# Kernel tuning notes

Hardware: AMD Instinct MI355X
Metric: run time of the kernel (lower is better)

The kernel has to match this reference:

```python
import jax, jax.numpy as jnp
import numpy as np

KRYLOV_DIM = 8
T_END = 1.0
EPS = 1e-12


def setup_inputs() -> dict:
    key = jax.random.key(0)
    k1, k2, k3 = jax.random.split(key, 3)
    B, C, H, Wd = 8, 256, 64, 64
    s0 = jax.random.uniform(k1, (B, C, H, Wd), dtype=jnp.float32)
    v = jax.random.normal(k2, (B, C, H, Wd), dtype=jnp.float32)
    W = jax.random.normal(k3, (C, C), dtype=jnp.float32) / np.float32(np.sqrt(C))
    return {"s0": s0, "v": v, "W": W}


def reference(s0, v, W):
    # fitness: learned channel-mixing linear operator (1x1-conv style)
    def fitness(x):
        return jnp.einsum('oc,bchw->bohw', W, x)

    # replicator vector field R_{s}[x] = s*x - s * sum_c(s*x)
    def replicator(s, x):
        sx = s * x
        return sx - s * jnp.sum(sx, axis=1, keepdims=True)

    A = lambda x: fitness(replicator(s0, x))
    dot = lambda a, b: jnp.sum(a * b, axis=(1, 2, 3))  # batched inner product

    m = KRYLOV_DIM
    B = v.shape[0]

    # ---- Arnoldi iteration (batched, modified Gram-Schmidt) ----
    vnorm = jnp.sqrt(dot(v, v))  # [B]
    Q = [v / vnorm[:, None, None, None]]
    Hcols = []
    for k in range(m):
        w = A(Q[k])
        col = []
        for j in range(k + 1):
            h = dot(Q[j], w)               # [B]
            col.append(h)
            w = w - h[:, None, None, None] * Q[j]
        hnext = jnp.sqrt(dot(w, w))        # subdiagonal entry
        Q.append(w / (hnext + EPS)[:, None, None, None])
        col.append(hnext)
        col += [jnp.zeros_like(hnext)] * (m - k - 1)  # pad column to m+1 rows
        Hcols.append(jnp.stack(col, axis=-1))          # [B, m+1]
    Hmat = jnp.stack(Hcols, axis=-1)  # [B, m+1, m]
    T = Hmat[:, :m, :]                # square upper-Hessenberg [B, m, m]

    # ---- extended matrix + batched small matrix exponential ----
    ext = jnp.zeros((B, m + 1, m + 1), dtype=T.dtype)
    ext = ext.at[:, :m, :m].set(T_END * T)
    ext = ext.at[:, 0, m].set(T_END)
    expm_ext = jax.scipy.linalg.expm(ext)   # batched over leading dim
    coords = expm_ext[:, :m, -1]            # [B, m] Krylov coordinates

    # ---- fused weighted sum of Krylov vectors ----
    Qstack = jnp.stack(Q[:m], axis=0)       # [m, B, C, H, W]
    v_end = jnp.einsum('bj,jbchw->bchw', coords, Qstack)
    return v_end * vnorm[:, None, None, None]
```

## Files before the change

kernel.cpp:

```cpp
#include <hip/hip_runtime.h>
#include <math.h>

#define Bn   8
#define Cn   256
#define HWn  4096
#define FB   (Cn * HWn)
#define NTOT (Bn * FB)
#define TEND 1.0
#define EPSK 1e-12f
#define NT   64
#define RS   56
#define WTS  68

typedef float f32x4 __attribute__((ext_vector_type(4)));
typedef short bf16x8 __attribute__((ext_vector_type(8)));

__device__ inline float b2f(unsigned int u) {
    return __uint_as_float(u << 16);
}
__device__ inline unsigned short f2b(float f) {
    unsigned u = __float_as_uint(f);
    unsigned r = u + 0x7FFFu + ((u >> 16) & 1u);
    return (unsigned short)(r >> 16);
}


__global__ void init_kernel(float* __restrict__ p) {
    for (int i = threadIdx.x; i < 1024; i += 256) p[i] = 0.0f;
}

__global__ void wsplit_kernel(const float* __restrict__ W,
                              unsigned short* __restrict__ Whs,
                              unsigned short* __restrict__ Wls) {
    int kc = blockIdx.x, mt = blockIdx.y, l = threadIdx.x;
    int m = mt * 16 + (l & 15);
    int k0 = kc * 32 + (l >> 4) * 8;
#pragma unroll
    for (int j = 0; j < 8; ++j) {
        float wv = W[m * 256 + k0 + j];
        unsigned short h = f2b(wv);
        unsigned short lo = f2b(wv - b2f(h));
        int idx = ((kc * 16 + mt) * 64 + l) * 8 + j;
        Whs[idx] = h; Wls[idx] = lo;
    }
}

template <int K>
__global__ __launch_bounds__(256, 3) void step_kernel(
        const float* __restrict__ v, const float* __restrict__ s0,
        const unsigned short* __restrict__ Whs, const unsigned short* __restrict__ Wls,
        unsigned short* __restrict__ Qb, float* __restrict__ acc,
        float* __restrict__ w) {
    __shared__ __align__(16) char smem_u[34816];
    short* Ph   = (short*)smem_u;
    short* Pl   = (short*)(smem_u + 7168);
    float* tred = (float*)(smem_u + 14336);
    float* wt   = (float*)smem_u;
    __shared__ float ts[NT];
    __shared__ float nred[4];
    __shared__ float dred[4][8];
    const int tid = threadIdx.x;
    const int b = blockIdx.y;
    const int sbase = blockIdx.x * NT;
    const size_t boff = (size_t)b * FB;
    const int lane = tid & 63, wvi = tid >> 6;
    const int mbase = wvi * 64;
    const int cg = tid >> 4;
    const int pos = (tid & 15) * 4;

    float cj[K > 0 ? K : 1];
    if (K > 0) {
        float mm[K > 0 ? K : 1];
        mm[0] = sqrtf(acc[512 + b]);
#pragma unroll
        for (int j = 1; j < K; ++j) mm[j] = sqrtf(acc[512 + j * 8 + b]) + EPSK * mm[j - 1];
#pragma unroll
        for (int j = 0; j < K; ++j)
            cj[j] = acc[((K - 1) * 8 + j) * 8 + b] / (mm[j] * mm[j]);
    }
    unsigned short* QK = Qb + (size_t)(K > 0 ? K - 1 : 0) * NTOT;

    float tp[4] = {0.f, 0.f, 0.f, 0.f};
    float np = 0.f;
#pragma unroll 4
    for (int cc = 0; cc < 16; ++cc) {
        int c = cc * 16 + cg;
        size_t off = boff + (size_t)c * HWn + sbase + pos;
        float4 sv = *(const float4*)(s0 + off);
        float se[4] = {sv.x, sv.y, sv.z, sv.w};
        if (K == 0) {
            float4 xv = *(const float4*)(v + off);
            float xe[4] = {xv.x, xv.y, xv.z, xv.w};
#pragma unroll
            for (int i = 0; i < 4; ++i) {
                np = fmaf(xe[i], xe[i], np);
                tp[i] = fmaf(xe[i], se[i], tp[i]);
            }
        } else {
            float4 wv4 = *(const float4*)(w + off);
            float4 vv4 = *(const float4*)(v + off);
            float xe[4];
            xe[0] = fmaf(-cj[0], vv4.x, wv4.x);
            xe[1] = fmaf(-cj[0], vv4.y, wv4.y);
            xe[2] = fmaf(-cj[0], vv4.z, wv4.z);
            xe[3] = fmaf(-cj[0], vv4.w, wv4.w);
#pragma unroll
            for (int j = 1; j < K; ++j) {
                ushort4 u = *(const ushort4*)(Qb + (size_t)(j - 1) * NTOT + off);
                xe[0] = fmaf(-cj[j], b2f(u.x), xe[0]);
                xe[1] = fmaf(-cj[j], b2f(u.y), xe[1]);
                xe[2] = fmaf(-cj[j], b2f(u.z), xe[2]);
                xe[3] = fmaf(-cj[j], b2f(u.w), xe[3]);
            }
            unsigned int h0 = f2b(xe[0]), h1 = f2b(xe[1]);
            unsigned int h2 = f2b(xe[2]), h3 = f2b(xe[3]);
            ushort4 o;
            o.x = (unsigned short)h0; o.y = (unsigned short)h1;
            o.z = (unsigned short)h2; o.w = (unsigned short)h3;
            *(ushort4*)(QK + off) = o;
            float xr[4] = {b2f(h0), b2f(h1), b2f(h2), b2f(h3)};
#pragma unroll
            for (int i = 0; i < 4; ++i) {
                np = fmaf(xr[i], xr[i], np);
                tp[i] = fmaf(xr[i], se[i], tp[i]);
            }
        }
    }
    for (int off2 = 32; off2 > 0; off2 >>= 1) np += __shfl_down(np, off2);
    if (lane == 0) nred[wvi] = np;
    *(float4*)(tred + cg * WTS + pos) = *(float4*)tp;
    __syncthreads();
    if (tid < 64) {
        float s = 0.f;
#pragma unroll
        for (int g = 0; g < 16; ++g) s += tred[g * WTS + tid];
        ts[tid] = s;
    }
    if (tid == 0)
        atomicAdd(&acc[512 + K * 8 + b], nred[0] + nred[1] + nred[2] + nred[3]);
    __syncthreads();

    f32x4 ac[4][4];
#pragma unroll
    for (int i = 0; i < 4; ++i)
#pragma unroll
        for (int j = 0; j < 4; ++j) ac[i][j] = (f32x4){0.f, 0.f, 0.f, 0.f};

    for (int kc = 0; kc < 8; ++kc) {
        __syncthreads();
#pragma unroll
        for (int ci = 0; ci < 2; ++ci) {
            int cl = ci * 16 + cg;
            int c = kc * 32 + cl;
            size_t off = boff + (size_t)c * HWn + sbase + pos;
            float4 sv = *(const float4*)(s0 + off);
            float se[4] = {sv.x, sv.y, sv.z, sv.w};
            float xr[4];
            if (K == 0) {
                float4 xv = *(const float4*)(v + off);
                xr[0] = xv.x; xr[1] = xv.y; xr[2] = xv.z; xr[3] = xv.w;
            } else {
                ushort4 u = *(const ushort4*)(QK + off);
                xr[0] = b2f(u.x); xr[1] = b2f(u.y); xr[2] = b2f(u.z); xr[3] = b2f(u.w);
            }
#pragma unroll
            for (int i = 0; i < 4; ++i) {
                float p = se[i] * (xr[i] - ts[pos + i]);
                unsigned short h = f2b(p);
                unsigned short l = f2b(p - b2f(h));
                Ph[(pos + i) * RS + cl] = (short)h;
                Pl[(pos + i) * RS + cl] = (short)l;
            }
        }
        __syncthreads();
        bf16x8 ah[4], al[4], bh[4], bl[4];
#pragma unroll
        for (int rt = 0; rt < 4; ++rt) {
            int mt = (mbase >> 4) + rt;
            ah[rt] = *(const bf16x8*)(Whs + (size_t)kc * 8192 + (mt * 64 + lane) * 8);
            al[rt] = *(const bf16x8*)(Wls + (size_t)kc * 8192 + (mt * 64 + lane) * 8);
        }
#pragma unroll
        for (int ct = 0; ct < 4; ++ct) {
            int n = ct * 16 + (lane & 15);
            int k8 = (lane >> 4) * 8;
            bh[ct] = *(bf16x8*)(Ph + n * RS + k8);
            bl[ct] = *(bf16x8*)(Pl + n * RS + k8);
        }
#pragma unroll
        for (int rt = 0; rt < 4; ++rt)
#pragma unroll
            for (int ct = 0; ct < 4; ++ct) {
                ac[rt][ct] = __builtin_amdgcn_mfma_f32_16x16x32_bf16(ah[rt], bh[ct], ac[rt][ct], 0, 0, 0);
                ac[rt][ct] = __builtin_amdgcn_mfma_f32_16x16x32_bf16(ah[rt], bl[ct], ac[rt][ct], 0, 0, 0);
                ac[rt][ct] = __builtin_amdgcn_mfma_f32_16x16x32_bf16(al[rt], bh[ct], ac[rt][ct], 0, 0, 0);
            }
    }

    float dp[K + 1];
#pragma unroll
    for (int j = 0; j <= K; ++j) dp[j] = 0.f;
#pragma unroll
    for (int g = 0; g < 2; ++g) {
        __syncthreads();
        if ((wvi >> 1) == g) {
            int rl = (wvi & 1) * 64;
#pragma unroll
            for (int rt = 0; rt < 4; ++rt)
#pragma unroll
                for (int ct = 0; ct < 4; ++ct) {
                    int r0 = rl + rt * 16 + (lane >> 4) * 4;
                    int ccol = ct * 16 + (lane & 15);
#pragma unroll
                    for (int reg = 0; reg < 4; ++reg)
                        wt[(r0 + reg) * WTS + ccol] = ac[rt][ct][reg];
                }
        }
        __syncthreads();
#pragma unroll
        for (int rr = 0; rr < 8; ++rr) {
            int rlocal = rr * 16 + (tid >> 4);
            int rabs = g * 128 + rlocal;
            int col = (tid & 15) * 4;
            const float* src = wt + rlocal * WTS + col;
            float4 wv4 = {src[0], src[1], src[2], src[3]};
            size_t idx = boff + (size_t)rabs * HWn + sbase + col;
            *(float4*)(w + idx) = wv4;
            float4 vv4 = *(const float4*)(v + idx);
            dp[0] = fmaf(wv4.x, vv4.x, dp[0]);
            dp[0] = fmaf(wv4.y, vv4.y, dp[0]);
            dp[0] = fmaf(wv4.z, vv4.z, dp[0]);
            dp[0] = fmaf(wv4.w, vv4.w, dp[0]);
#pragma unroll
            for (int j = 1; j <= K; ++j) {
                ushort4 u = *(const ushort4*)(Qb + (size_t)(j - 1) * NTOT + idx);
                dp[j] = fmaf(wv4.x, b2f(u.x), dp[j]);
                dp[j] = fmaf(wv4.y, b2f(u.y), dp[j]);
                dp[j] = fmaf(wv4.z, b2f(u.z), dp[j]);
                dp[j] = fmaf(wv4.w, b2f(u.w), dp[j]);
            }
        }
    }
#pragma unroll
    for (int j = 0; j <= K; ++j) {
        float q = dp[j];
        for (int off2 = 32; off2 > 0; off2 >>= 1) q += __shfl_down(q, off2);
        if (lane == 0) dred[wvi][j] = q;
    }
    __syncthreads();
    if (tid <= K)
        atomicAdd(&acc[(K * 8 + tid) * 8 + b],
                  dred[0][tid] + dred[1][tid] + dred[2][tid] + dred[3][tid]);
}

__global__ __launch_bounds__(128) void expm_kernel(const float* __restrict__ acc,
                                                   float* __restrict__ coordsOut) {
    __shared__ double Am[81], Pm[81], Tm[81];
    __shared__ double ssc;
    __shared__ int sn;
    const int b = blockIdx.x;
    const int t = threadIdx.x;
    const int r = t / 9, c = t % 9;
    double m[8];
    m[0] = sqrt((double)acc[512 + b]);
    for (int j = 1; j < 8; ++j) m[j] = sqrt((double)acc[512 + j * 8 + b]) + 1e-12 * m[j - 1];
    if (t < 81) {
        double val = 0.0;
        if (r < 8 && c < 8) {
            if (r <= c) val = TEND * (double)acc[(c * 8 + r) * 8 + b] / (m[r] * m[c]);
            else if (r == c + 1) val = TEND * sqrt((double)acc[512 + r * 8 + b]) / m[c];
        }
        if (r == 0 && c == 8) val = TEND;
        Am[t] = val;
    }
    __syncthreads();
    if (t == 0) {
        double mx = 0.0;
        for (int rr = 0; rr < 9; ++rr) {
            double s = 0.0;
            for (int cc = 0; cc < 9; ++cc) s += fabs(Am[rr * 9 + cc]);
            if (s > mx) mx = s;
        }
        int n = 0;
        while (mx > 0.25 && n < 48) { mx *= 0.5; ++n; }
        double sc = 1.0;
        for (int ii = 0; ii < n; ++ii) sc *= 0.5;
        sn = n; ssc = sc;
    }
    __syncthreads();
    if (t < 81) Am[t] *= ssc;
    __syncthreads();
    if (t < 81) Pm[t] = (r == c) ? 1.0 : 0.0;
    __syncthreads();
    for (int i = 20; i >= 1; --i) {
        if (t < 81) {
            double s = 0.0;
            for (int k = 0; k < 9; ++k) s += Am[r * 9 + k] * Pm[k * 9 + c];
            Tm[t] = ((r == c) ? 1.0 : 0.0) + s / (double)i;
        }
        __syncthreads();
        if (t < 81) Pm[t] = Tm[t];
        __syncthreads();
    }
    int n = sn;
    for (int q = 0; q < n; ++q) {
        if (t < 81) {
            double s = 0.0;
            for (int k = 0; k < 9; ++k) s += Pm[r * 9 + k] * Pm[k * 9 + c];
            Tm[t] = s;
        }
        __syncthreads();
        if (t < 81) Pm[t] = Tm[t];
        __syncthreads();
    }
    if (t < 8) coordsOut[b * 8 + t] = (float)(Pm[t * 9 + 8] * m[0] / m[t]);
}

__device__ inline void unp8(uint4 u, float* f) {
    f[0] = b2f(u.x & 0xFFFFu); f[1] = b2f(u.x >> 16);
    f[2] = b2f(u.y & 0xFFFFu); f[3] = b2f(u.y >> 16);
    f[4] = b2f(u.z & 0xFFFFu); f[5] = b2f(u.z >> 16);
    f[6] = b2f(u.w & 0xFFFFu); f[7] = b2f(u.w >> 16);
}

__global__ __launch_bounds__(256) void combine_kernel(const unsigned short* __restrict__ Qb,
                                                      const float* __restrict__ v,
                                                      const float* __restrict__ coords,
                                                      float* __restrict__ out) {
    int b = blockIdx.y;
    const size_t boff = (size_t)b * FB;
    float cf[8];
#pragma unroll
    for (int j = 0; j < 8; ++j) cf[j] = coords[b * 8 + j];
    const float4* vv = (const float4*)(v + boff);
    const uint4* uv[8];
#pragma unroll
    for (int j = 1; j < 8; ++j)
        uv[j] = (const uint4*)(Qb + (size_t)(j - 1) * NTOT + boff);
    int i = blockIdx.x * 256 + threadIdx.x;
    float4* ov = (float4*)(out + boff);
#pragma unroll
    for (int r = 0; r < 2; ++r) {
        int idx = i + r * 65536;
        float4 v0 = vv[2 * idx], v1 = vv[2 * idx + 1];
        float a[8] = {cf[0] * v0.x, cf[0] * v0.y, cf[0] * v0.z, cf[0] * v0.w,
                      cf[0] * v1.x, cf[0] * v1.y, cf[0] * v1.z, cf[0] * v1.w};
#pragma unroll
        for (int j = 1; j < 8; ++j) {
            uint4 u = uv[j][idx];
            float ue[8]; unp8(u, ue);
#pragma unroll
            for (int e = 0; e < 8; ++e) a[e] = fmaf(cf[j], ue[e], a[e]);
        }
        float4 o0 = {a[0], a[1], a[2], a[3]};
        float4 o1 = {a[4], a[5], a[6], a[7]};
        ov[2 * idx] = o0; ov[2 * idx + 1] = o1;
    }
}

extern "C" void kernel_launch(void* const* d_in, const int* in_sizes, int n_in,
                              void* d_out, int out_size, void* d_ws, size_t ws_size,
                              hipStream_t stream) {
    const float* s0 = (const float*)d_in[0];
    const float* v  = (const float*)d_in[1];
    const float* W  = (const float*)d_in[2];
    float* out = (float*)d_out;

    float* ws     = (float*)d_ws;
    float* acc    = ws;
    float* coords = ws + 576;
    unsigned short* Whs = (unsigned short*)(ws + 1024);
    unsigned short* Wls = (unsigned short*)(ws + 1024 + 32768);
    unsigned short* Qb  = (unsigned short*)(ws + 1024 + 65536);
    float* w      = out;

    init_kernel<<<dim3(1), dim3(256), 0, stream>>>(ws);
    wsplit_kernel<<<dim3(8, 16), dim3(64), 0, stream>>>(W, Whs, Wls);

    dim3 ga(64, 8), blk(256);
#define STEPK(K) step_kernel<K><<<ga, blk, 0, stream>>>(v, s0, Whs, Wls, Qb, acc, w);
    STEPK(0) STEPK(1) STEPK(2) STEPK(3) STEPK(4) STEPK(5) STEPK(6) STEPK(7)
#undef STEPK

    expm_kernel<<<dim3(8), dim3(128), 0, stream>>>(acc, coords);
    combine_kernel<<<dim3(256, 8), blk, 0, stream>>>(Qb, v, coords, out);
}
```

Before: 541.6 us.

## Halve spatial tile and double-buffer the staged operand in LDS

The spatial tile per block drops from 64 to 32 positions, doubling the grid to 128x8 blocks and raising the launch-bounds occupancy target from 3 to 4. The bf16 hi/lo operand staging is double-buffered, so the next channel chunk is built while MFMAs run on the current one, removing one barrier per k-step. The epilogue now writes the whole accumulator tile at once instead of in two halves. The smaller tile gives less reuse of the W fragments per block, which are reloaded twice as often in total.

```diff
diff --git a/kernel.cpp b/kernel.cpp
--- a/kernel.cpp
+++ b/kernel.cpp
@@ -8,9 +8,10 @@
 #define NTOT (Bn * FB)
 #define TEND 1.0
 #define EPSK 1e-12f
-#define NT   64
-#define RS   56
-#define WTS  68
+#define NT   32
+#define RS   40
+#define TS   36
+#define WTS  36
 
 typedef float f32x4 __attribute__((ext_vector_type(4)));
 typedef short bf16x8 __attribute__((ext_vector_type(8)));
@@ -46,15 +47,17 @@
 }
 
 template <int K>
-__global__ __launch_bounds__(256, 3) void step_kernel(
+__global__ __launch_bounds__(256, 4) void step_kernel(
         const float* __restrict__ v, const float* __restrict__ s0,
         const unsigned short* __restrict__ Whs, const unsigned short* __restrict__ Wls,
         unsigned short* __restrict__ Qb, float* __restrict__ acc,
         float* __restrict__ w) {
-    __shared__ __align__(16) char smem_u[34816];
-    short* Ph   = (short*)smem_u;
-    short* Pl   = (short*)(smem_u + 7168);
-    float* tred = (float*)(smem_u + 14336);
+    __shared__ __align__(16) char smem_u[36864];
+    short* Ph0  = (short*)smem_u;
+    short* Ph1  = (short*)(smem_u + 2560);
+    short* Pl0  = (short*)(smem_u + 5120);
+    short* Pl1  = (short*)(smem_u + 7680);
+    float* tred = (float*)(smem_u + 10240);
     float* wt   = (float*)smem_u;
     __shared__ float ts[NT];
     __shared__ float nred[4];
@@ -65,8 +68,8 @@
     const size_t boff = (size_t)b * FB;
     const int lane = tid & 63, wvi = tid >> 6;
     const int mbase = wvi * 64;
-    const int cg = tid >> 4;
-    const int pos = (tid & 15) * 4;
+    const int cg = tid >> 3;
+    const int pos = (tid & 7) * 4;
 
     float cj[K > 0 ? K : 1];
     if (K > 0) {
@@ -82,9 +85,9 @@
 
     float tp[4] = {0.f, 0.f, 0.f, 0.f};
     float np = 0.f;
-#pragma unroll 4
-    for (int cc = 0; cc < 16; ++cc) {
-        int c = cc * 16 + cg;
+#pragma unroll
+    for (int cc = 0; cc < 8; ++cc) {
+        int c = cc * 32 + cg;
         size_t off = boff + (size_t)c * HWn + sbase + pos;
         float4 sv = *(const float4*)(s0 + off);
         float se[4] = {sv.x, sv.y, sv.z, sv.w};
@@ -128,52 +131,55 @@
     }
     for (int off2 = 32; off2 > 0; off2 >>= 1) np += __shfl_down(np, off2);
     if (lane == 0) nred[wvi] = np;
-    *(float4*)(tred + cg * WTS + pos) = *(float4*)tp;
-    __syncthreads();
-    if (tid < 64) {
+    *(float4*)(tred + cg * TS + pos) = *(float4*)tp;
+    __syncthreads();
+    if (tid < NT) {
         float s = 0.f;
 #pragma unroll
-        for (int g = 0; g < 16; ++g) s += tred[g * WTS + tid];
+        for (int g = 0; g < 32; ++g) s += tred[g * TS + tid];
         ts[tid] = s;
     }
     if (tid == 0)
         atomicAdd(&acc[512 + K * 8 + b], nred[0] + nred[1] + nred[2] + nred[3]);
     __syncthreads();
 
-    f32x4 ac[4][4];
+    f32x4 ac[4][2];
 #pragma unroll
     for (int i = 0; i < 4; ++i)
 #pragma unroll
-        for (int j = 0; j < 4; ++j) ac[i][j] = (f32x4){0.f, 0.f, 0.f, 0.f};
-
+        for (int j = 0; j < 2; ++j) ac[i][j] = (f32x4){0.f, 0.f, 0.f, 0.f};
+
+    auto stage = [&](int kc, int bb) {
+        int c = kc * 32 + cg;
+        size_t off = boff + (size_t)c * HWn + sbase + pos;
+        float4 sv = *(const float4*)(s0 + off);
+        float se[4] = {sv.x, sv.y, sv.z, sv.w};
+        float xr[4];
+        if (K == 0) {
+            float4 xv = *(const float4*)(v + off);
+            xr[0] = xv.x; xr[1] = xv.y; xr[2] = xv.z; xr[3] = xv.w;
+        } else {
+            ushort4 u = *(const ushort4*)(QK + off);
+            xr[0] = b2f(u.x); xr[1] = b2f(u.y); xr[2] = b2f(u.z); xr[3] = b2f(u.w);
+        }
+        short* ph = bb ? Ph1 : Ph0;
+        short* pl = bb ? Pl1 : Pl0;
+#pragma unroll
+        for (int i = 0; i < 4; ++i) {
+            float p = se[i] * (xr[i] - ts[pos + i]);
+            unsigned short h = f2b(p);
+            unsigned short l = f2b(p - b2f(h));
+            ph[(pos + i) * RS + cg] = (short)h;
+            pl[(pos + i) * RS + cg] = (short)l;
+        }
+    };
+    stage(0, 0);
     for (int kc = 0; kc < 8; ++kc) {
         __syncthreads();
-#pragma unroll
-        for (int ci = 0; ci < 2; ++ci) {
-            int cl = ci * 16 + cg;
-            int c = kc * 32 + cl;
-            size_t off = boff + (size_t)c * HWn + sbase + pos;
-            float4 sv = *(const float4*)(s0 + off);
-            float se[4] = {sv.x, sv.y, sv.z, sv.w};
-            float xr[4];
-            if (K == 0) {
-                float4 xv = *(const float4*)(v + off);
-                xr[0] = xv.x; xr[1] = xv.y; xr[2] = xv.z; xr[3] = xv.w;
-            } else {
-                ushort4 u = *(const ushort4*)(QK + off);
-                xr[0] = b2f(u.x); xr[1] = b2f(u.y); xr[2] = b2f(u.z); xr[3] = b2f(u.w);
-            }
-#pragma unroll
-            for (int i = 0; i < 4; ++i) {
-                float p = se[i] * (xr[i] - ts[pos + i]);
-                unsigned short h = f2b(p);
-                unsigned short l = f2b(p - b2f(h));
-                Ph[(pos + i) * RS + cl] = (short)h;
-                Pl[(pos + i) * RS + cl] = (short)l;
-            }
-        }
-        __syncthreads();
-        bf16x8 ah[4], al[4], bh[4], bl[4];
+        if (kc < 7) stage(kc + 1, (kc + 1) & 1);
+        const short* ph = (kc & 1) ? Ph1 : Ph0;
+        const short* pl = (kc & 1) ? Pl1 : Pl0;
+        bf16x8 ah[4], al[4], bh[2], bl[2];
 #pragma unroll
         for (int rt = 0; rt < 4; ++rt) {
             int mt = (mbase >> 4) + rt;
@@ -181,64 +187,57 @@
             al[rt] = *(const bf16x8*)(Wls + (size_t)kc * 8192 + (mt * 64 + lane) * 8);
         }
 #pragma unroll
-        for (int ct = 0; ct < 4; ++ct) {
+        for (int ct = 0; ct < 2; ++ct) {
             int n = ct * 16 + (lane & 15);
             int k8 = (lane >> 4) * 8;
-            bh[ct] = *(bf16x8*)(Ph + n * RS + k8);
-            bl[ct] = *(bf16x8*)(Pl + n * RS + k8);
+            bh[ct] = *(const bf16x8*)(ph + n * RS + k8);
+            bl[ct] = *(const bf16x8*)(pl + n * RS + k8);
         }
 #pragma unroll
         for (int rt = 0; rt < 4; ++rt)
 #pragma unroll
-            for (int ct = 0; ct < 4; ++ct) {
+            for (int ct = 0; ct < 2; ++ct) {
                 ac[rt][ct] = __builtin_amdgcn_mfma_f32_16x16x32_bf16(ah[rt], bh[ct], ac[rt][ct], 0, 0, 0);
                 ac[rt][ct] = __builtin_amdgcn_mfma_f32_16x16x32_bf16(ah[rt], bl[ct], ac[rt][ct], 0, 0, 0);
                 ac[rt][ct] = __builtin_amdgcn_mfma_f32_16x16x32_bf16(al[rt], bh[ct], ac[rt][ct], 0, 0, 0);
             }
     }
 
+    __syncthreads();
+#pragma unroll
+    for (int rt = 0; rt < 4; ++rt)
+#pragma unroll
+        for (int ct = 0; ct < 2; ++ct) {
+            int r0 = mbase + rt * 16 + (lane >> 4) * 4;
+            int col = ct * 16 + (lane & 15);
+#pragma unroll
+            for (int reg = 0; reg < 4; ++reg)
+                wt[(r0 + reg) * WTS + col] = ac[rt][ct][reg];
+        }
+    __syncthreads();
     float dp[K + 1];
 #pragma unroll
     for (int j = 0; j <= K; ++j) dp[j] = 0.f;
 #pragma unroll
-    for (int g = 0; g < 2; ++g) {
-        __syncthreads();
-        if ((wvi >> 1) == g) {
-            int rl = (wvi & 1) * 64;
-#pragma unroll
-            for (int rt = 0; rt < 4; ++rt)
-#pragma unroll
-                for (int ct = 0; ct < 4; ++ct) {
-                    int r0 = rl + rt * 16 + (lane >> 4) * 4;
-                    int ccol = ct * 16 + (lane & 15);
-#pragma unroll
-                    for (int reg = 0; reg < 4; ++reg)
-                        wt[(r0 + reg) * WTS + ccol] = ac[rt][ct][reg];
-                }
-        }
-        __syncthreads();
-#pragma unroll
-        for (int rr = 0; rr < 8; ++rr) {
-            int rlocal = rr * 16 + (tid >> 4);
-            int rabs = g * 128 + rlocal;
-            int col = (tid & 15) * 4;
-            const float* src = wt + rlocal * WTS + col;
-            float4 wv4 = {src[0], src[1], src[2], src[3]};
-            size_t idx = boff + (size_t)rabs * HWn + sbase + col;
-            *(float4*)(w + idx) = wv4;
-            float4 vv4 = *(const float4*)(v + idx);
-            dp[0] = fmaf(wv4.x, vv4.x, dp[0]);
-            dp[0] = fmaf(wv4.y, vv4.y, dp[0]);
-            dp[0] = fmaf(wv4.z, vv4.z, dp[0]);
-            dp[0] = fmaf(wv4.w, vv4.w, dp[0]);
-#pragma unroll
-            for (int j = 1; j <= K; ++j) {
-                ushort4 u = *(const ushort4*)(Qb + (size_t)(j - 1) * NTOT + idx);
-                dp[j] = fmaf(wv4.x, b2f(u.x), dp[j]);
-                dp[j] = fmaf(wv4.y, b2f(u.y), dp[j]);
-                dp[j] = fmaf(wv4.z, b2f(u.z), dp[j]);
-                dp[j] = fmaf(wv4.w, b2f(u.w), dp[j]);
-            }
+    for (int rr = 0; rr < 8; ++rr) {
+        int rabs = rr * 32 + (tid >> 3);
+        int col = (tid & 7) * 4;
+        const float* src = wt + rabs * WTS + col;
+        float4 wv4 = {src[0], src[1], src[2], src[3]};
+        size_t idx = boff + (size_t)rabs * HWn + sbase + col;
+        *(float4*)(w + idx) = wv4;
+        float4 vv4 = *(const float4*)(v + idx);
+        dp[0] = fmaf(wv4.x, vv4.x, dp[0]);
+        dp[0] = fmaf(wv4.y, vv4.y, dp[0]);
+        dp[0] = fmaf(wv4.z, vv4.z, dp[0]);
+        dp[0] = fmaf(wv4.w, vv4.w, dp[0]);
+#pragma unroll
+        for (int j = 1; j <= K; ++j) {
+            ushort4 u = *(const ushort4*)(Qb + (size_t)(j - 1) * NTOT + idx);
+            dp[j] = fmaf(wv4.x, b2f(u.x), dp[j]);
+            dp[j] = fmaf(wv4.y, b2f(u.y), dp[j]);
+            dp[j] = fmaf(wv4.z, b2f(u.z), dp[j]);
+            dp[j] = fmaf(wv4.w, b2f(u.w), dp[j]);
         }
     }
 #pragma unroll
@@ -377,7 +376,7 @@
     init_kernel<<<dim3(1), dim3(256), 0, stream>>>(ws);
     wsplit_kernel<<<dim3(8, 16), dim3(64), 0, stream>>>(W, Whs, Wls);
 
-    dim3 ga(64, 8), blk(256);
+    dim3 ga(128, 8), blk(256);
 #define STEPK(K) step_kernel<K><<<ga, blk, 0, stream>>>(v, s0, Whs, Wls, Qb, acc, w);
     STEPK(0) STEPK(1) STEPK(2) STEPK(3) STEPK(4) STEPK(5) STEPK(6) STEPK(7)
 #undef STEPK
```

Result: slower. 665.5 us (+22.9%).

## Precompute W·s0 once and fold the replicator mean term in after the GEMM

Applied to the files above, without the earlier changes.

The replicator operator is split algebraically: W(s⊙x) − (W s0)·t, where t is the per-pixel channel sum of s⊙x. A new K=-1 launch computes Z = W·s0 once and stores it as bf16 hi/lo pairs. Each Arnoldi step then stages s⊙x straight into a double-buffered LDS tile, with no separate first pass over all channels to compute t before the GEMM, and subtracts Z·t in the epilogue. This removes one full read sweep per step and overlaps staging with the MFMAs. The cost is an extra GEMM launch, extra Z reads per step, more workspace, an occupancy hint lowered from 3 to 2 blocks, and some precision risk from reconstructing Z out of bf16 parts.

```diff
diff --git a/kernel.cpp b/kernel.cpp
--- a/kernel.cpp
+++ b/kernel.cpp
@@ -9,7 +9,7 @@
 #define TEND 1.0
 #define EPSK 1e-12f
 #define NT   64
-#define RS   56
+#define RS   40
 #define WTS  68
 
 typedef float f32x4 __attribute__((ext_vector_type(4)));
@@ -46,27 +46,31 @@
 }
 
 template <int K>
-__global__ __launch_bounds__(256, 3) void step_kernel(
+__global__ __launch_bounds__(256, 2) void step_kernel(
         const float* __restrict__ v, const float* __restrict__ s0,
         const unsigned short* __restrict__ Whs, const unsigned short* __restrict__ Wls,
         unsigned short* __restrict__ Qb, float* __restrict__ acc,
-        float* __restrict__ w) {
+        float* __restrict__ w,
+        unsigned short* __restrict__ Zh, unsigned short* __restrict__ Zl) {
     __shared__ __align__(16) char smem_u[34816];
-    short* Ph   = (short*)smem_u;
-    short* Pl   = (short*)(smem_u + 7168);
-    float* tred = (float*)(smem_u + 14336);
-    float* wt   = (float*)smem_u;
+    short* Ph0 = (short*)smem_u;
+    short* Ph1 = (short*)(smem_u + 5120);
+    short* Pl0 = (short*)(smem_u + 10240);
+    short* Pl1 = (short*)(smem_u + 15360);
+    float* wt  = (float*)smem_u;
+    __shared__ float tred[4][64];
     __shared__ float ts[NT];
     __shared__ float nred[4];
     __shared__ float dred[4][8];
+
     const int tid = threadIdx.x;
     const int b = blockIdx.y;
     const int sbase = blockIdx.x * NT;
     const size_t boff = (size_t)b * FB;
     const int lane = tid & 63, wvi = tid >> 6;
     const int mbase = wvi * 64;
-    const int cg = tid >> 4;
-    const int pos = (tid & 15) * 4;
+    const int ch8 = wvi * 8;
+    const int p   = lane;
 
     float cj[K > 0 ? K : 1];
     if (K > 0) {
@@ -80,65 +84,46 @@
     }
     unsigned short* QK = Qb + (size_t)(K > 0 ? K - 1 : 0) * NTOT;
 
-    float tp[4] = {0.f, 0.f, 0.f, 0.f};
-    float np = 0.f;
-#pragma unroll 4
-    for (int cc = 0; cc < 16; ++cc) {
-        int c = cc * 16 + cg;
-        size_t off = boff + (size_t)c * HWn + sbase + pos;
-        float4 sv = *(const float4*)(s0 + off);
-        float se[4] = {sv.x, sv.y, sv.z, sv.w};
-        if (K == 0) {
-            float4 xv = *(const float4*)(v + off);
-            float xe[4] = {xv.x, xv.y, xv.z, xv.w};
-#pragma unroll
-            for (int i = 0; i < 4; ++i) {
-                np = fmaf(xe[i], xe[i], np);
-                tp[i] = fmaf(xe[i], se[i], tp[i]);
+    float tp = 0.f, np = 0.f;
+
+    auto stage = [&](int kc, int bb) {
+        const int c0 = kc * 32 + ch8;
+        const size_t off = boff + (size_t)c0 * HWn + sbase + p;
+        short* ph = bb ? Ph1 : Ph0;
+        short* pl = bb ? Pl1 : Pl0;
+        bf16x8 hv, lv;
+#pragma unroll
+        for (int e = 0; e < 8; ++e) {
+            const size_t oe = off + (size_t)e * HWn;
+            float s = s0[oe];
+            float pe;
+            if (K < 0) {
+                pe = s;
+            } else if (K == 0) {
+                float xv = v[oe];
+                np = fmaf(xv, xv, np);
+                tp = fmaf(xv, s, tp);
+                pe = s * xv;
+            } else {
+                float xe = w[oe];
+                xe = fmaf(-cj[0], v[oe], xe);
+#pragma unroll
+                for (int j = 1; j < K; ++j)
+                    xe = fmaf(-cj[j], b2f(Qb[(size_t)(j - 1) * NTOT + oe]), xe);
+                unsigned short hx = f2b(xe);
+                QK[oe] = hx;
+                float xr = b2f(hx);
+                np = fmaf(xr, xr, np);
+                tp = fmaf(xr, s, tp);
+                pe = s * xr;
             }
-        } else {
-            float4 wv4 = *(const float4*)(w + off);
-            float4 vv4 = *(const float4*)(v + off);
-            float xe[4];
-            xe[0] = fmaf(-cj[0], vv4.x, wv4.x);
-            xe[1] = fmaf(-cj[0], vv4.y, wv4.y);
-            xe[2] = fmaf(-cj[0], vv4.z, wv4.z);
-            xe[3] = fmaf(-cj[0], vv4.w, wv4.w);
-#pragma unroll
-            for (int j = 1; j < K; ++j) {
-                ushort4 u = *(const ushort4*)(Qb + (size_t)(j - 1) * NTOT + off);
-                xe[0] = fmaf(-cj[j], b2f(u.x), xe[0]);
-                xe[1] = fmaf(-cj[j], b2f(u.y), xe[1]);
-                xe[2] = fmaf(-cj[j], b2f(u.z), xe[2]);
-                xe[3] = fmaf(-cj[j], b2f(u.w), xe[3]);
-            }
-            unsigned int h0 = f2b(xe[0]), h1 = f2b(xe[1]);
-            unsigned int h2 = f2b(xe[2]), h3 = f2b(xe[3]);
-            ushort4 o;
-            o.x = (unsigned short)h0; o.y = (unsigned short)h1;
-            o.z = (unsigned short)h2; o.w = (unsigned short)h3;
-            *(ushort4*)(QK + off) = o;
-            float xr[4] = {b2f(h0), b2f(h1), b2f(h2), b2f(h3)};
-#pragma unroll
-            for (int i = 0; i < 4; ++i) {
-                np = fmaf(xr[i], xr[i], np);
-                tp[i] = fmaf(xr[i], se[i], tp[i]);
-            }
-        }
-    }
-    for (int off2 = 32; off2 > 0; off2 >>= 1) np += __shfl_down(np, off2);
-    if (lane == 0) nred[wvi] = np;
-    *(float4*)(tred + cg * WTS + pos) = *(float4*)tp;
-    __syncthreads();
-    if (tid < 64) {
-        float s = 0.f;
-#pragma unroll
-        for (int g = 0; g < 16; ++g) s += tred[g * WTS + tid];
-        ts[tid] = s;
-    }
-    if (tid == 0)
-        atomicAdd(&acc[512 + K * 8 + b], nred[0] + nred[1] + nred[2] + nred[3]);
-    __syncthreads();
+            unsigned short h = f2b(pe);
+            hv[e] = (short)h;
+            lv[e] = (short)f2b(pe - b2f(h));
+        }
+        *(bf16x8*)(ph + p * RS + ch8) = hv;
+        *(bf16x8*)(pl + p * RS + ch8) = lv;
+    };
 
     f32x4 ac[4][4];
 #pragma unroll
@@ -146,33 +131,12 @@
 #pragma unroll
         for (int j = 0; j < 4; ++j) ac[i][j] = (f32x4){0.f, 0.f, 0.f, 0.f};
 
+    stage(0, 0);
     for (int kc = 0; kc < 8; ++kc) {
         __syncthreads();
-#pragma unroll
-        for (int ci = 0; ci < 2; ++ci) {
-            int cl = ci * 16 + cg;
-            int c = kc * 32 + cl;
-            size_t off = boff + (size_t)c * HWn + sbase + pos;
-            float4 sv = *(const float4*)(s0 + off);
-            float se[4] = {sv.x, sv.y, sv.z, sv.w};
-            float xr[4];
-            if (K == 0) {
-                float4 xv = *(const float4*)(v + off);
-                xr[0] = xv.x; xr[1] = xv.y; xr[2] = xv.z; xr[3] = xv.w;
-            } else {
-                ushort4 u = *(const ushort4*)(QK + off);
-                xr[0] = b2f(u.x); xr[1] = b2f(u.y); xr[2] = b2f(u.z); xr[3] = b2f(u.w);
-            }
-#pragma unroll
-            for (int i = 0; i < 4; ++i) {
-                float p = se[i] * (xr[i] - ts[pos + i]);
-                unsigned short h = f2b(p);
-                unsigned short l = f2b(p - b2f(h));
-                Ph[(pos + i) * RS + cl] = (short)h;
-                Pl[(pos + i) * RS + cl] = (short)l;
-            }
-        }
-        __syncthreads();
+        if (kc < 7) stage(kc + 1, (kc + 1) & 1);
+        const short* ph = (kc & 1) ? Ph1 : Ph0;
+        const short* pl = (kc & 1) ? Pl1 : Pl0;
         bf16x8 ah[4], al[4], bh[4], bl[4];
 #pragma unroll
         for (int rt = 0; rt < 4; ++rt) {
@@ -184,8 +148,8 @@
         for (int ct = 0; ct < 4; ++ct) {
             int n = ct * 16 + (lane & 15);
             int k8 = (lane >> 4) * 8;
-            bh[ct] = *(bf16x8*)(Ph + n * RS + k8);
-            bl[ct] = *(bf16x8*)(Pl + n * RS + k8);
+            bh[ct] = *(const bf16x8*)(ph + n * RS + k8);
+            bl[ct] = *(const bf16x8*)(pl + n * RS + k8);
         }
 #pragma unroll
         for (int rt = 0; rt < 4; ++rt)
@@ -197,9 +161,24 @@
             }
     }
 
-    float dp[K + 1];
-#pragma unroll
-    for (int j = 0; j <= K; ++j) dp[j] = 0.f;
+    __syncthreads();
+    if (K >= 0) {
+        tred[wvi][p] = tp;
+        float q = np;
+        for (int off2 = 32; off2 > 0; off2 >>= 1) q += __shfl_down(q, off2);
+        if (lane == 0) nred[wvi] = q;
+    }
+    __syncthreads();
+    if (K >= 0) {
+        if (tid < NT)
+            ts[tid] = tred[0][tid] + tred[1][tid] + tred[2][tid] + tred[3][tid];
+        if (tid == 0)
+            atomicAdd(&acc[512 + K * 8 + b], nred[0] + nred[1] + nred[2] + nred[3]);
+    }
+
+    float dp[K >= 0 ? K + 1 : 1];
+#pragma unroll
+    for (int j = 0; j < (K >= 0 ? K + 1 : 1); ++j) dp[j] = 0.f;
 #pragma unroll
     for (int g = 0; g < 2; ++g) {
         __syncthreads();
@@ -225,32 +204,54 @@
             const float* src = wt + rlocal * WTS + col;
             float4 wv4 = {src[0], src[1], src[2], src[3]};
             size_t idx = boff + (size_t)rabs * HWn + sbase + col;
-            *(float4*)(w + idx) = wv4;
-            float4 vv4 = *(const float4*)(v + idx);
-            dp[0] = fmaf(wv4.x, vv4.x, dp[0]);
-            dp[0] = fmaf(wv4.y, vv4.y, dp[0]);
-            dp[0] = fmaf(wv4.z, vv4.z, dp[0]);
-            dp[0] = fmaf(wv4.w, vv4.w, dp[0]);
-#pragma unroll
-            for (int j = 1; j <= K; ++j) {
-                ushort4 u = *(const ushort4*)(Qb + (size_t)(j - 1) * NTOT + idx);
-                dp[j] = fmaf(wv4.x, b2f(u.x), dp[j]);
-                dp[j] = fmaf(wv4.y, b2f(u.y), dp[j]);
-                dp[j] = fmaf(wv4.z, b2f(u.z), dp[j]);
-                dp[j] = fmaf(wv4.w, b2f(u.w), dp[j]);
+            if (K < 0) {
+                ushort4 zh4, zl4;
+                unsigned short h0 = f2b(wv4.x), h1 = f2b(wv4.y);
+                unsigned short h2 = f2b(wv4.z), h3 = f2b(wv4.w);
+                zh4.x = h0; zh4.y = h1; zh4.z = h2; zh4.w = h3;
+                zl4.x = f2b(wv4.x - b2f(h0)); zl4.y = f2b(wv4.y - b2f(h1));
+                zl4.z = f2b(wv4.z - b2f(h2)); zl4.w = f2b(wv4.w - b2f(h3));
+                *(ushort4*)(Zh + idx) = zh4;
+                *(ushort4*)(Zl + idx) = zl4;
+            } else {
+                ushort4 zh4 = *(const ushort4*)(Zh + idx);
+                ushort4 zl4 = *(const ushort4*)(Zl + idx);
+                float z0 = b2f(zh4.x) + b2f(zl4.x), z1 = b2f(zh4.y) + b2f(zl4.y);
+                float z2 = b2f(zh4.z) + b2f(zl4.z), z3 = b2f(zh4.w) + b2f(zl4.w);
+                float4 wf;
+                wf.x = wv4.x - z0 * ts[col + 0];
+                wf.y = wv4.y - z1 * ts[col + 1];
+                wf.z = wv4.z - z2 * ts[col + 2];
+                wf.w = wv4.w - z3 * ts[col + 3];
+                *(float4*)(w + idx) = wf;
+                float4 vv4 = *(const float4*)(v + idx);
+                dp[0] = fmaf(wf.x, vv4.x, dp[0]);
+                dp[0] = fmaf(wf.y, vv4.y, dp[0]);
+                dp[0] = fmaf(wf.z, vv4.z, dp[0]);
+                dp[0] = fmaf(wf.w, vv4.w, dp[0]);
+#pragma unroll
+                for (int j = 1; j <= (K >= 0 ? K : 0); ++j) {
+                    ushort4 u = *(const ushort4*)(Qb + (size_t)(j - 1) * NTOT + idx);
+                    dp[j] = fmaf(wf.x, b2f(u.x), dp[j]);
+                    dp[j] = fmaf(wf.y, b2f(u.y), dp[j]);
+                    dp[j] = fmaf(wf.z, b2f(u.z), dp[j]);
+                    dp[j] = fmaf(wf.w, b2f(u.w), dp[j]);
+                }
             }
         }
     }
-#pragma unroll
-    for (int j = 0; j <= K; ++j) {
-        float q = dp[j];
-        for (int off2 = 32; off2 > 0; off2 >>= 1) q += __shfl_down(q, off2);
-        if (lane == 0) dred[wvi][j] = q;
-    }
-    __syncthreads();
-    if (tid <= K)
-        atomicAdd(&acc[(K * 8 + tid) * 8 + b],
-                  dred[0][tid] + dred[1][tid] + dred[2][tid] + dred[3][tid]);
+    if (K >= 0) {
+#pragma unroll
+        for (int j = 0; j <= K; ++j) {
+            float q = dp[j];
+            for (int off2 = 32; off2 > 0; off2 >>= 1) q += __shfl_down(q, off2);
+            if (lane == 0) dred[wvi][j] = q;
+        }
+        __syncthreads();
+        if (tid <= K)
+            atomicAdd(&acc[(K * 8 + tid) * 8 + b],
+                      dred[0][tid] + dred[1][tid] + dred[2][tid] + dred[3][tid]);
+    }
 }
 
 __global__ __launch_bounds__(128) void expm_kernel(const float* __restrict__ acc,
@@ -370,15 +371,18 @@
     float* acc    = ws;
     float* coords = ws + 576;
     unsigned short* Whs = (unsigned short*)(ws + 1024);
-    unsigned short* Wls = (unsigned short*)(ws + 1024 + 32768);
-    unsigned short* Qb  = (unsigned short*)(ws + 1024 + 65536);
+    unsigned short* Wls = Whs + 65536;
+    unsigned short* Zh  = (unsigned short*)(ws + 1024 + 65536);
+    unsigned short* Zl  = Zh + NTOT;
+    unsigned short* Qb  = Zh + 2 * (size_t)NTOT;
     float* w      = out;
 
     init_kernel<<<dim3(1), dim3(256), 0, stream>>>(ws);
     wsplit_kernel<<<dim3(8, 16), dim3(64), 0, stream>>>(W, Whs, Wls);
 
     dim3 ga(64, 8), blk(256);
-#define STEPK(K) step_kernel<K><<<ga, blk, 0, stream>>>(v, s0, Whs, Wls, Qb, acc, w);
+    step_kernel<-1><<<ga, blk, 0, stream>>>(v, s0, Whs, Wls, Qb, acc, w, Zh, Zl);
+#define STEPK(K) step_kernel<K><<<ga, blk, 0, stream>>>(v, s0, Whs, Wls, Qb, acc, w, Zh, Zl);
     STEPK(0) STEPK(1) STEPK(2) STEPK(3) STEPK(4) STEPK(5) STEPK(6) STEPK(7)
 #undef STEPK
 
```

After: 579.1 us. +6.9%, slower.
